# Optimization experiments

Measured on AMD Instinct MI355X. Metric: run time of the kernel, lower is better.

## Reference

```python
import jax, jax.numpy as jnp
import numpy as np
from jax import lax

T, B, IN, H, L, OUT = 2048, 64, 512, 256, 3, 2

def setup_inputs() -> dict:
    key = jax.random.key(0)
    ks = list(jax.random.split(key, 4 * L + 3))
    d = {"x": jax.random.normal(ks[0], (T, B, IN), jnp.float32)}
    s_in = 1.0 / np.sqrt(H)
    for l in range(L):
        fin = IN if l == 0 else H
        d[f"w_ih_{l}"] = jax.random.uniform(ks[1 + 4 * l], (H, fin), jnp.float32, -s_in, s_in)
        d[f"w_hh_{l}"] = jax.random.uniform(ks[2 + 4 * l], (H, H), jnp.float32, -s_in, s_in)
        d[f"b_ih_{l}"] = jax.random.uniform(ks[3 + 4 * l], (H,), jnp.float32, -s_in, s_in)
        d[f"b_hh_{l}"] = jax.random.uniform(ks[4 + 4 * l], (H,), jnp.float32, -s_in, s_in)
    d["w_out"] = jax.random.uniform(ks[-2], (OUT, H), jnp.float32, -s_in, s_in)
    d["b_out"] = jax.random.uniform(ks[-1], (OUT,), jnp.float32, -s_in, s_in)
    return d

def _rnn_layer(xs, w_ih, w_hh, b_ih, b_hh):
    # xs: (T, B, F); precompute input projection, scan the recurrence
    pre = jnp.einsum('tbf,hf->tbh', xs, w_ih) + b_ih + b_hh  # (T,B,H)
    h0 = jnp.zeros((xs.shape[1], w_hh.shape[0]), xs.dtype)
    def step(h, p):
        h = jnp.tanh(p + h @ w_hh.T)
        return h, h
    _, hs = lax.scan(step, h0, pre)
    return hs  # (T, B, H)

def reference(x, w_ih_0, w_hh_0, b_ih_0, b_hh_0, w_ih_1, w_hh_1, b_ih_1, b_hh_1,
              w_ih_2, w_hh_2, b_ih_2, b_hh_2, w_out, b_out):
    params = [(w_ih_0, w_hh_0, b_ih_0, b_hh_0),
              (w_ih_1, w_hh_1, b_ih_1, b_hh_1),
              (w_ih_2, w_hh_2, b_ih_2, b_hh_2)]
    h = x
    for w_ih, w_hh, b_ih, b_hh in params:
        h = _rnn_layer(h, w_ih, w_hh, b_ih, b_hh)
    # Faithful to source: r_out[:, -1, :] selects last BATCH element over all timesteps
    feat = h[:, -1, :]                      # (T, H)
    out = feat @ w_out.T + b_out            # (T, OUT)
    return out[:, None, :]                  # (T, 1, OUT)
```

## Files before the change

kernel.cpp:

```cpp
#include <hip/hip_runtime.h>
#include <hip/hip_bf16.h>


#define T_STEPS 2048
#define B_SZ    64
#define IN_F    512
#define H_SZ    256
#define OUT_F   2
#define CHUNK   16
#define NCHUNK  (T_STEPS / CHUNK)

#define REP32(M) M(0) M(1) M(2) M(3) M(4) M(5) M(6) M(7) \
                 M(8) M(9) M(10) M(11) M(12) M(13) M(14) M(15) \
                 M(16) M(17) M(18) M(19) M(20) M(21) M(22) M(23) \
                 M(24) M(25) M(26) M(27) M(28) M(29) M(30) M(31)

#define W_DECL(n) const float4 wq##n = wrow[n];
#define W_FMA(n)  { float4 hv = hv4[n];                \
                    a0 = fmaf(wq##n.x, hv.x, a0);      \
                    a1 = fmaf(wq##n.y, hv.y, a1);      \
                    a2 = fmaf(wq##n.z, hv.z, a2);      \
                    a3 = fmaf(wq##n.w, hv.w, a3); }

__device__ __forceinline__ float fast_tanh(float x) {
    float e = __expf(2.f * x);
    return 1.f - 2.f / (e + 1.f);
}

__device__ __forceinline__ void wait_ge(int* flag, int target) {
    if (threadIdx.x == 0) {
        while (__hip_atomic_load(flag, __ATOMIC_ACQUIRE, __HIP_MEMORY_SCOPE_AGENT) < target)
            __builtin_amdgcn_s_sleep(1);
    }
    __syncthreads();
}

__device__ __forceinline__ void post_flag(int* flag, int val) {
    __threadfence();
    __syncthreads();
    if (threadIdx.x == 0)
        __hip_atomic_store(flag, val, __ATOMIC_RELEASE, __HIP_MEMORY_SCOPE_AGENT);
}

__device__ void scan_stage(const float* __restrict__ pre, const float* __restrict__ Whh,
                           float* __restrict__ Hout, int* wait_f, int* post_f)
{
    __shared__ __align__(16) float h2[2][H_SZ];
    __shared__ __align__(16) float ps[CHUNK][H_SZ];
    const int tid = threadIdx.x;
    const int j = tid >> 1;
    const int p = tid & 1;

    const float4* wrow = (const float4*)(Whh + j * H_SZ + p * 128);
    REP32(W_DECL)

    if (tid < H_SZ) h2[0][tid] = 0.f;
    __syncthreads();

    int buf = 0;
    for (int c = 0; c < NCHUNK; ++c) {
        if (wait_f) wait_ge(wait_f, c + 1);

        {
            const float4* src = (const float4*)(pre + (size_t)c * CHUNK * H_SZ);
            float4* dst = (float4*)&ps[0][0];
            dst[tid]       = src[tid];
            dst[tid + 512] = src[tid + 512];
        }
        __syncthreads();

        #pragma unroll 1
        for (int r = 0; r < CHUNK; ++r) {
            const float4* hv4 = (const float4*)(h2[buf] + p * 128);
            float a0 = 0.f, a1 = 0.f, a2 = 0.f, a3 = 0.f;
            REP32(W_FMA)
            float acc = (a0 + a1) + (a2 + a3);
            acc += __shfl_xor(acc, 1);
            float hn = fast_tanh(ps[r][j] + acc);
            if (p == 0) {
                h2[buf ^ 1][j] = hn;
                Hout[(size_t)(c * CHUNK + r) * H_SZ + j] = hn;
            }
            __syncthreads();
            buf ^= 1;
        }
        if (post_f) post_flag(post_f, c + 1);
    }
}

__device__ void ih_stage(const float* __restrict__ Hin, const float* __restrict__ Wih,
                         const float* __restrict__ b1, const float* __restrict__ b2,
                         float* __restrict__ PREout, int* wait_f, int* post_f)
{
    __shared__ __align__(16) float xs[CHUNK][H_SZ];
    const int tid = threadIdx.x;
    const int j = tid >> 1;
    const int p = tid & 1;

    const float4* wrow = (const float4*)(Wih + j * H_SZ + p * 128);
    REP32(W_DECL)

    const float bb = b1[j] + b2[j];

    for (int c = 0; c < NCHUNK; ++c) {
        wait_ge(wait_f, c + 1);
        {
            const float4* src = (const float4*)(Hin + (size_t)c * CHUNK * H_SZ);
            float4* dst = (float4*)&xs[0][0];
            dst[tid]       = src[tid];
            dst[tid + 512] = src[tid + 512];
        }
        __syncthreads();

        #pragma unroll 1
        for (int r = 0; r < CHUNK; ++r) {
            const float4* hv4 = (const float4*)(xs[r] + p * 128);
            float a0 = 0.f, a1 = 0.f, a2 = 0.f, a3 = 0.f;
            REP32(W_FMA)
            float acc = (a0 + a1) + (a2 + a3);
            acc += __shfl_xor(acc, 1);
            if (p == 0)
                PREout[(size_t)(c * CHUNK + r) * H_SZ + j] = acc + bb;
        }
        post_flag(post_f, c + 1);
    }
}

__device__ void out_stage(const float* __restrict__ Hs, const float* __restrict__ Wout,
                          const float* __restrict__ bout, float* __restrict__ out,
                          int* wait_f)
{
    const int tid = threadIdx.x;
    const int wv = tid >> 6;
    const int l  = tid & 63;

    const float w00 = Wout[l];
    const float w01 = Wout[l + 64];
    const float w02 = Wout[l + 128];
    const float w03 = Wout[l + 192];
    const float w10 = Wout[H_SZ + l];
    const float w11 = Wout[H_SZ + l + 64];
    const float w12 = Wout[H_SZ + l + 128];
    const float w13 = Wout[H_SZ + l + 192];
    const float b0 = bout[0], b1 = bout[1];

    for (int c = 0; c < NCHUNK; ++c) {
        wait_ge(wait_f, c + 1);
        #pragma unroll
        for (int s = 0; s < 2; ++s) {
            const int t = c * CHUNK + wv * 2 + s;
            const float* hrow = Hs + (size_t)t * H_SZ;
            float h0 = hrow[l], h1 = hrow[l + 64], h2 = hrow[l + 128], h3 = hrow[l + 192];
            float a0 = fmaf(h0, w00, fmaf(h1, w01, fmaf(h2, w02, h3 * w03)));
            float a1 = fmaf(h0, w10, fmaf(h1, w11, fmaf(h2, w12, h3 * w13)));
            #pragma unroll
            for (int sh = 32; sh; sh >>= 1) {
                a0 += __shfl_xor(a0, sh);
                a1 += __shfl_xor(a1, sh);
            }
            if (l == 0) {
                out[t * OUT_F + 0] = a0 + b0;
                out[t * OUT_F + 1] = a1 + b1;
            }
        }
    }
}

__global__ __launch_bounds__(512, 1)
void pipeline_kernel(const float* __restrict__ PRE0,
                     const float* __restrict__ w_hh0, const float* __restrict__ w_hh1,
                     const float* __restrict__ w_hh2,
                     const float* __restrict__ w_ih1, const float* __restrict__ w_ih2,
                     const float* __restrict__ b_ih1, const float* __restrict__ b_hh1,
                     const float* __restrict__ b_ih2, const float* __restrict__ b_hh2,
                     const float* __restrict__ w_out, const float* __restrict__ b_out,
                     float* __restrict__ H0, float* __restrict__ H1, float* __restrict__ H2,
                     float* __restrict__ PRE1, float* __restrict__ PRE2,
                     float* __restrict__ out, int* __restrict__ flags)
{
    switch (blockIdx.x) {
    case 0: scan_stage(PRE0, w_hh0, H0, nullptr,   flags + 0); break;
    case 1: ih_stage(H0, w_ih1, b_ih1, b_hh1, PRE1, flags + 0, flags + 1); break;
    case 2: scan_stage(PRE1, w_hh1, H1, flags + 1, flags + 2); break;
    case 3: ih_stage(H1, w_ih2, b_ih2, b_hh2, PRE2, flags + 2, flags + 3); break;
    case 4: scan_stage(PRE2, w_hh2, H2, flags + 3, flags + 4); break;
    case 5: out_stage(H2, w_out, b_out, out, flags + 4); break;
    }
}

__global__ __launch_bounds__(512)
void pre_gemm_kernel(const float* __restrict__ in,
                     const float* __restrict__ W,
                     const float* __restrict__ b1, const float* __restrict__ b2,
                     float* __restrict__ pre)
{
    __shared__ __align__(16) float xs[8][IN_F];
    const int tid = threadIdx.x;
    const int j = tid >> 1;
    const int p = tid & 1;
    const long t0 = (long)blockIdx.x * 8;

    for (int idx = tid; idx < 8 * (IN_F / 4); idx += 512) {
        const int r = idx >> 7;
        const int q = idx & 127;
        const float4* srow = (const float4*)(in + (t0 + r) * ((long)B_SZ * IN_F)
                                                + (long)(B_SZ - 1) * IN_F);
        ((float4*)xs[r])[q] = srow[q];
    }
    __syncthreads();

    float acc[8] = {0.f, 0.f, 0.f, 0.f, 0.f, 0.f, 0.f, 0.f};
    const float4* wr = (const float4*)(W + (long)j * IN_F + p * (IN_F / 2));
    #pragma unroll 2
    for (int q = 0; q < IN_F / 8; ++q) {
        float4 wv = wr[q];
        #pragma unroll
        for (int r = 0; r < 8; ++r) {
            float4 xv = ((const float4*)(xs[r] + p * (IN_F / 2)))[q];
            acc[r] = fmaf(wv.x, xv.x, acc[r]);
            acc[r] = fmaf(wv.y, xv.y, acc[r]);
            acc[r] = fmaf(wv.z, xv.z, acc[r]);
            acc[r] = fmaf(wv.w, xv.w, acc[r]);
        }
    }
    const float bb = b1[j] + b2[j];
    #pragma unroll
    for (int r = 0; r < 8; ++r) {
        float v = acc[r] + __shfl_xor(acc[r], 1);
        if (p == 0)
            pre[(t0 + r) * H_SZ + j] = v + bb;
    }
}

extern "C" void kernel_launch(void* const* d_in, const int* in_sizes, int n_in,
                              void* d_out, int out_size, void* d_ws, size_t ws_size,
                              hipStream_t stream)
{
    const float* x     = (const float*)d_in[0];
    const float* w_ih0 = (const float*)d_in[1];
    const float* w_hh0 = (const float*)d_in[2];
    const float* b_ih0 = (const float*)d_in[3];
    const float* b_hh0 = (const float*)d_in[4];
    const float* w_ih1 = (const float*)d_in[5];
    const float* w_hh1 = (const float*)d_in[6];
    const float* b_ih1 = (const float*)d_in[7];
    const float* b_hh1 = (const float*)d_in[8];
    const float* w_ih2 = (const float*)d_in[9];
    const float* w_hh2 = (const float*)d_in[10];
    const float* b_ih2 = (const float*)d_in[11];
    const float* b_hh2 = (const float*)d_in[12];
    const float* w_out = (const float*)d_in[13];
    const float* b_out = (const float*)d_in[14];
    float* out = (float*)d_out;

    const size_t TH = (size_t)T_STEPS * H_SZ;
    float* PRE0 = (float*)d_ws;
    float* PRE1 = PRE0 + TH;
    float* PRE2 = PRE1 + TH;
    float* H0   = PRE2 + TH;
    float* H1   = H0 + TH;
    float* H2   = H1 + TH;
    int* flags  = (int*)(H2 + TH);

    hipMemsetAsync(flags, 0, 8 * sizeof(int), stream);

    pre_gemm_kernel<<<T_STEPS / 8, 512, 0, stream>>>(x, w_ih0, b_ih0, b_hh0, PRE0);

    pipeline_kernel<<<6, 512, 0, stream>>>(PRE0, w_hh0, w_hh1, w_hh2,
                                           w_ih1, w_ih2,
                                           b_ih1, b_hh1, b_ih2, b_hh2,
                                           w_out, b_out,
                                           H0, H1, H2, PRE1, PRE2,
                                           out, flags);
}
```

Baseline: 2.889 ms.

## Retile recurrent matvec to 4 rows x 8 segments per thread with rotated LDS reads

Changes the thread mapping in the scan and input-projection stages. Each thread now computes 4 output rows over a 32-column segment instead of one row over half the columns, so every LDS hidden-state vector read feeds four rows of FMAs. Segment offsets are rotated per thread to avoid LDS bank conflicts, the 8-lane partials are combined with a butterfly shuffle, and results are stored as float4. Weights are pinned in registers with empty asm and the launch bound becomes waves_per_eu(2,2), which risks register pressure and a longer dependent FMA chain per step.

```diff
diff --git a/kernel.cpp b/kernel.cpp
--- a/kernel.cpp
+++ b/kernel.cpp
@@ -10,17 +10,9 @@
 #define CHUNK   16
 #define NCHUNK  (T_STEPS / CHUNK)
 
-#define REP32(M) M(0) M(1) M(2) M(3) M(4) M(5) M(6) M(7) \
-                 M(8) M(9) M(10) M(11) M(12) M(13) M(14) M(15) \
-                 M(16) M(17) M(18) M(19) M(20) M(21) M(22) M(23) \
-                 M(24) M(25) M(26) M(27) M(28) M(29) M(30) M(31)
-
-#define W_DECL(n) const float4 wq##n = wrow[n];
-#define W_FMA(n)  { float4 hv = hv4[n];                \
-                    a0 = fmaf(wq##n.x, hv.x, a0);      \
-                    a1 = fmaf(wq##n.y, hv.y, a1);      \
-                    a2 = fmaf(wq##n.z, hv.z, a2);      \
-                    a3 = fmaf(wq##n.w, hv.w, a3); }
+typedef __attribute__((ext_vector_type(4))) float f32x4;
+
+#define REP8(M) M(0) M(1) M(2) M(3) M(4) M(5) M(6) M(7)
 
 __device__ __forceinline__ float fast_tanh(float x) {
     float e = __expf(2.f * x);
@@ -42,17 +34,47 @@
         __hip_atomic_store(flag, val, __ATOMIC_RELEASE, __HIP_MEMORY_SCOPE_AGENT);
 }
 
+#define RO_DECL(i) const int ro##i = (((seg + i) & 7) << 2);
+
+#define W_DECL(i) \
+    f32x4 w0_##i = *(const f32x4*)(wbase + 0 * H_SZ + ro##i); \
+    f32x4 w1_##i = *(const f32x4*)(wbase + 1 * H_SZ + ro##i); \
+    f32x4 w2_##i = *(const f32x4*)(wbase + 2 * H_SZ + ro##i); \
+    f32x4 w3_##i = *(const f32x4*)(wbase + 3 * H_SZ + ro##i);
+
+#define W_PIN8(a0,a1,a2,a3,a4,a5,a6,a7) \
+    asm volatile("" : "+v"(a0), "+v"(a1), "+v"(a2), "+v"(a3), \
+                      "+v"(a4), "+v"(a5), "+v"(a6), "+v"(a7));
+#define W_PIN_ALL \
+    W_PIN8(w0_0, w0_1, w0_2, w0_3, w0_4, w0_5, w0_6, w0_7) \
+    W_PIN8(w1_0, w1_1, w1_2, w1_3, w1_4, w1_5, w1_6, w1_7) \
+    W_PIN8(w2_0, w2_1, w2_2, w2_3, w2_4, w2_5, w2_6, w2_7) \
+    W_PIN8(w3_0, w3_1, w3_2, w3_3, w3_4, w3_5, w3_6, w3_7)
+
+#define TILE_FMA(i) { \
+    const f32x4 hq = *(const f32x4*)(hb + ro##i); \
+    a0 = fmaf(w0_##i.x, hq.x, fmaf(w0_##i.y, hq.y, fmaf(w0_##i.z, hq.z, fmaf(w0_##i.w, hq.w, a0)))); \
+    a1 = fmaf(w1_##i.x, hq.x, fmaf(w1_##i.y, hq.y, fmaf(w1_##i.z, hq.z, fmaf(w1_##i.w, hq.w, a1)))); \
+    a2 = fmaf(w2_##i.x, hq.x, fmaf(w2_##i.y, hq.y, fmaf(w2_##i.z, hq.z, fmaf(w2_##i.w, hq.w, a2)))); \
+    a3 = fmaf(w3_##i.x, hq.x, fmaf(w3_##i.y, hq.y, fmaf(w3_##i.z, hq.z, fmaf(w3_##i.w, hq.w, a3)))); }
+
+#define BFLY_REDUCE \
+    a0 += __shfl_xor(a0, 1); a1 += __shfl_xor(a1, 1); a2 += __shfl_xor(a2, 1); a3 += __shfl_xor(a3, 1); \
+    a0 += __shfl_xor(a0, 2); a1 += __shfl_xor(a1, 2); a2 += __shfl_xor(a2, 2); a3 += __shfl_xor(a3, 2); \
+    a0 += __shfl_xor(a0, 4); a1 += __shfl_xor(a1, 4); a2 += __shfl_xor(a2, 4); a3 += __shfl_xor(a3, 4);
+
 __device__ void scan_stage(const float* __restrict__ pre, const float* __restrict__ Whh,
                            float* __restrict__ Hout, int* wait_f, int* post_f)
 {
     __shared__ __align__(16) float h2[2][H_SZ];
     __shared__ __align__(16) float ps[CHUNK][H_SZ];
     const int tid = threadIdx.x;
-    const int j = tid >> 1;
-    const int p = tid & 1;
-
-    const float4* wrow = (const float4*)(Whh + j * H_SZ + p * 128);
-    REP32(W_DECL)
+    const int seg = tid & 7;
+    const int rb  = tid >> 3;
+
+    REP8(RO_DECL)
+    const float* wbase = Whh + (size_t)(rb << 2) * H_SZ + (seg << 5);
+    REP8(W_DECL)
 
     if (tid < H_SZ) h2[0][tid] = 0.f;
     __syncthreads();
@@ -60,10 +82,11 @@
     int buf = 0;
     for (int c = 0; c < NCHUNK; ++c) {
         if (wait_f) wait_ge(wait_f, c + 1);
+        W_PIN_ALL
 
         {
-            const float4* src = (const float4*)(pre + (size_t)c * CHUNK * H_SZ);
-            float4* dst = (float4*)&ps[0][0];
+            const f32x4* src = (const f32x4*)(pre + (size_t)c * CHUNK * H_SZ);
+            f32x4* dst = (f32x4*)&ps[0][0];
             dst[tid]       = src[tid];
             dst[tid + 512] = src[tid + 512];
         }
@@ -71,15 +94,19 @@
 
         #pragma unroll 1
         for (int r = 0; r < CHUNK; ++r) {
-            const float4* hv4 = (const float4*)(h2[buf] + p * 128);
+            const float* hb = &h2[buf][seg << 5];
             float a0 = 0.f, a1 = 0.f, a2 = 0.f, a3 = 0.f;
-            REP32(W_FMA)
-            float acc = (a0 + a1) + (a2 + a3);
-            acc += __shfl_xor(acc, 1);
-            float hn = fast_tanh(ps[r][j] + acc);
-            if (p == 0) {
-                h2[buf ^ 1][j] = hn;
-                Hout[(size_t)(c * CHUNK + r) * H_SZ + j] = hn;
+            REP8(TILE_FMA)
+            BFLY_REDUCE
+            if (seg == 0) {
+                const f32x4 pv = *(const f32x4*)&ps[r][rb << 2];
+                f32x4 hn;
+                hn.x = fast_tanh(a0 + pv.x);
+                hn.y = fast_tanh(a1 + pv.y);
+                hn.z = fast_tanh(a2 + pv.z);
+                hn.w = fast_tanh(a3 + pv.w);
+                *(f32x4*)&h2[buf ^ 1][rb << 2] = hn;
+                *(f32x4*)(Hout + (size_t)(c * CHUNK + r) * H_SZ + (rb << 2)) = hn;
             }
             __syncthreads();
             buf ^= 1;
@@ -94,19 +121,21 @@
 {
     __shared__ __align__(16) float xs[CHUNK][H_SZ];
     const int tid = threadIdx.x;
-    const int j = tid >> 1;
-    const int p = tid & 1;
-
-    const float4* wrow = (const float4*)(Wih + j * H_SZ + p * 128);
-    REP32(W_DECL)
-
-    const float bb = b1[j] + b2[j];
+    const int seg = tid & 7;
+    const int rb  = tid >> 3;
+
+    REP8(RO_DECL)
+    const float* wbase = Wih + (size_t)(rb << 2) * H_SZ + (seg << 5);
+    REP8(W_DECL)
+
+    const f32x4 bb = *(const f32x4*)(b1 + (rb << 2)) + *(const f32x4*)(b2 + (rb << 2));
 
     for (int c = 0; c < NCHUNK; ++c) {
         wait_ge(wait_f, c + 1);
+        W_PIN_ALL
         {
-            const float4* src = (const float4*)(Hin + (size_t)c * CHUNK * H_SZ);
-            float4* dst = (float4*)&xs[0][0];
+            const f32x4* src = (const f32x4*)(Hin + (size_t)c * CHUNK * H_SZ);
+            f32x4* dst = (f32x4*)&xs[0][0];
             dst[tid]       = src[tid];
             dst[tid + 512] = src[tid + 512];
         }
@@ -114,13 +143,18 @@
 
         #pragma unroll 1
         for (int r = 0; r < CHUNK; ++r) {
-            const float4* hv4 = (const float4*)(xs[r] + p * 128);
+            const float* hb = &xs[r][seg << 5];
             float a0 = 0.f, a1 = 0.f, a2 = 0.f, a3 = 0.f;
-            REP32(W_FMA)
-            float acc = (a0 + a1) + (a2 + a3);
-            acc += __shfl_xor(acc, 1);
-            if (p == 0)
-                PREout[(size_t)(c * CHUNK + r) * H_SZ + j] = acc + bb;
+            REP8(TILE_FMA)
+            BFLY_REDUCE
+            if (seg == 0) {
+                f32x4 pv;
+                pv.x = a0 + bb.x;
+                pv.y = a1 + bb.y;
+                pv.z = a2 + bb.z;
+                pv.w = a3 + bb.w;
+                *(f32x4*)(PREout + (size_t)(c * CHUNK + r) * H_SZ + (rb << 2)) = pv;
+            }
         }
         post_flag(post_f, c + 1);
     }
@@ -166,7 +200,7 @@
     }
 }
 
-__global__ __launch_bounds__(512, 1)
+__global__ __attribute__((amdgpu_waves_per_eu(2, 2))) __launch_bounds__(512)
 void pipeline_kernel(const float* __restrict__ PRE0,
                      const float* __restrict__ w_hh0, const float* __restrict__ w_hh1,
                      const float* __restrict__ w_hh2,
```

Result: faster. 2.512 ms (-13.1%).
